# Performance work log

Hardware: AMD Instinct MI355X
Metric: run time of the kernel (lower is better)

## Reference

```python
import jax, jax.numpy as jnp
import numpy as np

N_NODES = 100000
N_EDGES = 1600000
IN_FEATS = 128
N_HIDDEN = 128
N_CLASSES = 47


def setup_inputs() -> dict:
    key = jax.random.key(0)
    ks = jax.random.split(key, 12)
    def lin(k, fi, fo):
        s = 1.0 / np.sqrt(fi)
        return jax.random.uniform(k, (fi, fo), jnp.float32, -s, s)
    return {
        "x": jax.random.normal(ks[0], (N_NODES, IN_FEATS), jnp.float32),
        "src": jax.random.randint(ks[1], (N_EDGES,), 0, N_NODES, jnp.int32),
        "dst": jax.random.randint(ks[2], (N_EDGES,), 0, N_NODES, jnp.int32),
        "W_self0": lin(ks[3], IN_FEATS, N_HIDDEN),
        "W_neigh0": lin(ks[4], IN_FEATS, N_HIDDEN),
        "b0": jnp.zeros((N_HIDDEN,), jnp.float32),
        "W_self1": lin(ks[5], N_HIDDEN, N_HIDDEN),
        "W_neigh1": lin(ks[6], N_HIDDEN, N_HIDDEN),
        "b1": jnp.zeros((N_HIDDEN,), jnp.float32),
        "W_self2": lin(ks[7], N_HIDDEN, N_CLASSES),
        "W_neigh2": lin(ks[8], N_HIDDEN, N_CLASSES),
        "b2": jnp.zeros((N_CLASSES,), jnp.float32),
    }


def _sage_layer(h, src, dst, W_self, W_neigh, b):
    # DGL SAGEConv 'mean': fc_self(h_dst) + fc_neigh(mean of in-neighbor feats) + bias
    agg = jax.ops.segment_sum(h[src], dst, num_segments=N_NODES)  # [N, d]
    deg = jax.ops.segment_sum(jnp.ones((src.shape[0],), h.dtype), dst,
                              num_segments=N_NODES)
    h_neigh = agg / jnp.maximum(deg, 1.0)[:, None]
    return h @ W_self + h_neigh @ W_neigh + b


def reference(x, src, dst, W_self0, W_neigh0, b0, W_self1, W_neigh1, b1,
              W_self2, W_neigh2, b2):
    h = _sage_layer(x, src, dst, W_self0, W_neigh0, b0)
    h = jax.nn.relu(h)
    h = _sage_layer(h, src, dst, W_self1, W_neigh1, b1)
    h = jax.nn.relu(h)
    h = _sage_layer(h, src, dst, W_self2, W_neigh2, b2)
    return h
```

## Files before the change

### kernel.cpp

```cpp
#include <hip/hip_runtime.h>

#define NN 100000
#define NE 1600000
#define NBK 391
#define CHUNK 8192
#define NBLK ((NE + CHUNK - 1) / CHUNK)
#define MPAD 100096
#define NCAST4 (NN * 32)
#define CAST512 (NCAST4 / 512)
#define GBLK 2048
#define NPW ((NN + 8191) / 8192)

using bf16x8 = __attribute__((ext_vector_type(8))) short;
using f32x4  = __attribute__((ext_vector_type(4))) float;

static __device__ __forceinline__ unsigned short f2bf(float f) {
    unsigned int u = __float_as_uint(f);
    unsigned int r = (u + 0x7FFFu + ((u >> 16) & 1u)) >> 16;
    return (unsigned short)r;
}
static __device__ __forceinline__ float lo16(unsigned int u) {
    return __uint_as_float(u << 16);
}
static __device__ __forceinline__ float hi16(unsigned int u) {
    return __uint_as_float(u & 0xFFFF0000u);
}
static __device__ __forceinline__ unsigned int pk(float lo, float hi) {
    return ((unsigned int)f2bf(hi) << 16) | (unsigned int)f2bf(lo);
}


__global__ __launch_bounds__(256) void k_hist(const int* __restrict__ dst,
                                              int* __restrict__ ghist) {
    __shared__ int h[NBK];
    int b = blockIdx.x, t = threadIdx.x;
    for (int i = t; i < NBK; i += 256) h[i] = 0;
    __syncthreads();
    int beg = b * CHUNK, end = min(beg + CHUNK, NE);
    for (int i = beg + t; i < end; i += 256)
        atomicAdd(&h[dst[i] >> 8], 1);
    __syncthreads();
    for (int i = t; i < NBK; i += 256) ghist[b * NBK + i] = h[i];
}

__global__ __launch_bounds__(512) void k_basescan_prep(
        const int* __restrict__ ghist, int* __restrict__ boff, int* __restrict__ gbase,
        const float4* __restrict__ x4, ushort4* __restrict__ XB4,
        const float* __restrict__ Ws0, const float* __restrict__ Wn0,
        unsigned short* __restrict__ BT0,
        const float* __restrict__ Ws1, const float* __restrict__ Wn1,
        unsigned short* __restrict__ BT1,
        const float* __restrict__ Ws2, const float* __restrict__ Wn2,
        unsigned short* __restrict__ BT2) {
    __shared__ int s[512];
    int bid = blockIdx.x, t = threadIdx.x;
    if (bid == 0) {
        int tot = 0;
        if (t < NBK) {
#pragma unroll 4
            for (int blk = 0; blk < NBLK; ++blk) tot += ghist[blk * NBK + t];
        }
        s[t] = tot;
        __syncthreads();
        for (int o = 1; o < 512; o <<= 1) {
            int u = (t >= o) ? s[t - o] : 0;
            __syncthreads();
            s[t] += u;
            __syncthreads();
        }
        int base = s[t] - tot;
        if (t <= NBK) boff[t] = base;
        if (t < NBK) {
            int run = base;
            for (int blk = 0; blk < NBLK; ++blk) {
                int g = ghist[blk * NBK + t];
                gbase[blk * NBK + t] = run;
                run += g;
            }
        }
        return;
    }
    int pb = bid - 1;
    if (pb < CAST512) {
        int i = pb * 512 + t;
        float4 v = x4[i];
        ushort4 o;
        o.x = f2bf(v.x); o.y = f2bf(v.y); o.z = f2bf(v.z); o.w = f2bf(v.w);
        XB4[i] = o;
    } else if (pb < CAST512 + 64) {
        int idx = (pb - CAST512) * 512 + t;
        int k = idx >> 7, n = idx & 127;
        float v = (k < 128) ? Ws0[k * 128 + n] : Wn0[(k - 128) * 128 + n];
        BT0[n * 256 + k] = f2bf(v);
    } else if (pb < CAST512 + 128) {
        int idx = (pb - CAST512 - 64) * 512 + t;
        int k = idx >> 7, n = idx & 127;
        float v = (k < 128) ? Ws1[k * 128 + n] : Wn1[(k - 128) * 128 + n];
        BT1[n * 256 + k] = f2bf(v);
    } else {
        int idx = (pb - CAST512 - 128) * 512 + t;
        if (idx < 96 * 128) {
            int n = idx >> 7, k = idx & 127;
            float v = 0.f;
            if (n < 48) { if (n < 47) v = Ws2[k * 47 + n]; }
            else        { int cc = n - 48; if (cc < 47) v = Wn2[k * 47 + cc]; }
            BT2[n * 128 + k] = f2bf(v);
        }
    }
}

__global__ __launch_bounds__(256) void k_scatter(const int* __restrict__ src,
                                                 const int* __restrict__ dst,
                                                 const int* __restrict__ gbase,
                                                 unsigned int* __restrict__ eb) {
    __shared__ int cur[NBK];
    int b = blockIdx.x, t = threadIdx.x;
    for (int i = t; i < NBK; i += 256) cur[i] = gbase[b * NBK + i];
    __syncthreads();
    int beg = b * CHUNK, end = min(beg + CHUNK, NE);
    for (int i = beg + t; i < end; i += 256) {
        int d = dst[i];
        int p = atomicAdd(&cur[d >> 8], 1);
        eb[p] = ((unsigned int)(d & 255) << 24) | (unsigned int)src[i];
    }
}

__global__ __launch_bounds__(256) void k_csr(const unsigned int* __restrict__ eb,
                                             const int* __restrict__ boff,
                                             int* __restrict__ rp,
                                             int* __restrict__ col) {
    __shared__ int h[256];
    __shared__ int sc[256];
    __shared__ int cur[256];
    int b = blockIdx.x, t = threadIdx.x;
    h[t] = 0;
    __syncthreads();
    int beg = boff[b], end = boff[b + 1];
    for (int e = beg + t; e < end; e += 256)
        atomicAdd(&h[eb[e] >> 24], 1);
    __syncthreads();
    int c = h[t];
    sc[t] = c;
    __syncthreads();
    for (int o = 1; o < 256; o <<= 1) {
        int v = (t >= o) ? sc[t - o] : 0;
        __syncthreads();
        sc[t] += v;
        __syncthreads();
    }
    int excl = beg + sc[t] - c;
    int node = (b << 8) + t;
    if (node < NN) rp[node] = excl;
    if (node == NN - 1) rp[NN] = NE;
    cur[t] = excl;
    __syncthreads();
    for (int e = beg + t; e < end; e += 256) {
        unsigned int p = eb[e];
        int pos = atomicAdd(&cur[p >> 24], 1);
        col[pos] = (int)(p & 0xFFFFFFu);
    }
}


__global__ __launch_bounds__(256) void k_gather128(
        const uint4* __restrict__ hb4,
        const int* __restrict__ rp, const int* __restrict__ col,
        uint4* __restrict__ hnb4) {
    int wave = blockIdx.x * 4 + (threadIdx.x >> 6);
    int lane = threadIdx.x & 63;
    int q = lane >> 4, l16 = lane & 15;
    int n0 = wave * NPW;
    int n1 = min(n0 + NPW, NN);
    for (int node = n0; node < n1; ++node) {
        int beg = rp[node], end = rp[node + 1];
        float a0 = 0.f, a1 = 0.f, a2 = 0.f, a3 = 0.f;
        float a4 = 0.f, a5 = 0.f, a6 = 0.f, a7 = 0.f;
        float b0 = 0.f, b1 = 0.f, b2 = 0.f, b3 = 0.f;
        float b4 = 0.f, b5 = 0.f, b6 = 0.f, b7 = 0.f;
        int e = beg;
        for (; e + 8 <= end; e += 8) {
            int c0 = col[e + q];
            int c1 = col[e + 4 + q];
            uint4 v0 = hb4[(size_t)c0 * 16 + l16];
            uint4 v1 = hb4[(size_t)c1 * 16 + l16];
            a0 += lo16(v0.x); a1 += hi16(v0.x); a2 += lo16(v0.y); a3 += hi16(v0.y);
            a4 += lo16(v0.z); a5 += hi16(v0.z); a6 += lo16(v0.w); a7 += hi16(v0.w);
            b0 += lo16(v1.x); b1 += hi16(v1.x); b2 += lo16(v1.y); b3 += hi16(v1.y);
            b4 += lo16(v1.z); b5 += hi16(v1.z); b6 += lo16(v1.w); b7 += hi16(v1.w);
        }
        for (; e < end; e += 4) {
            if (e + q < end) {
                uint4 v = hb4[(size_t)col[e + q] * 16 + l16];
                a0 += lo16(v.x); a1 += hi16(v.x); a2 += lo16(v.y); a3 += hi16(v.y);
                a4 += lo16(v.z); a5 += hi16(v.z); a6 += lo16(v.w); a7 += hi16(v.w);
            }
        }
        float s0 = a0 + b0, s1 = a1 + b1, s2 = a2 + b2, s3 = a3 + b3;
        float s4 = a4 + b4, s5 = a5 + b5, s6 = a6 + b6, s7 = a7 + b7;
        s0 += __shfl_xor(s0, 16); s0 += __shfl_xor(s0, 32);
        s1 += __shfl_xor(s1, 16); s1 += __shfl_xor(s1, 32);
        s2 += __shfl_xor(s2, 16); s2 += __shfl_xor(s2, 32);
        s3 += __shfl_xor(s3, 16); s3 += __shfl_xor(s3, 32);
        s4 += __shfl_xor(s4, 16); s4 += __shfl_xor(s4, 32);
        s5 += __shfl_xor(s5, 16); s5 += __shfl_xor(s5, 32);
        s6 += __shfl_xor(s6, 16); s6 += __shfl_xor(s6, 32);
        s7 += __shfl_xor(s7, 16); s7 += __shfl_xor(s7, 32);
        if (q == 0) {
            float d = (float)(end - beg);
            float inv = (d > 0.f) ? 1.0f / d : 0.0f;
            uint4 o;
            o.x = pk(s0 * inv, s1 * inv);
            o.y = pk(s2 * inv, s3 * inv);
            o.z = pk(s4 * inv, s5 * inv);
            o.w = pk(s6 * inv, s7 * inv);
            hnb4[(size_t)node * 16 + l16] = o;
        }
    }
}


__global__ __launch_bounds__(256, 2) void k_mgemm(
        const unsigned short* __restrict__ A0,
        const unsigned short* __restrict__ A1,
        const unsigned short* __restrict__ BT,
        const float* __restrict__ bias,
        unsigned short* __restrict__ outB) {
    int t = threadIdx.x;
    int lane = t & 63, wid = t >> 6;
    int wm = wid >> 1, wn = wid & 1;
    int lr = lane & 15, lg = lane >> 4;
    int row0 = blockIdx.x * 128 + wm * 64;
    int colw = wn * 64;
    f32x4 zero = {0.f, 0.f, 0.f, 0.f};
    f32x4 acc[4][4];
#pragma unroll
    for (int a = 0; a < 4; ++a)
#pragma unroll
        for (int b = 0; b < 4; ++b) acc[a][b] = zero;

#pragma unroll
    for (int p = 0; p < 2; ++p) {
        const unsigned short* A = p ? A1 : A0;
        bf16x8 bReg[4][4];
#pragma unroll
        for (int nf = 0; nf < 4; ++nf)
#pragma unroll
            for (int ks = 0; ks < 4; ++ks)
                bReg[nf][ks] = *(const bf16x8*)&BT[(size_t)(colw + nf * 16 + lr) * 256 + p * 128 + ks * 32 + lg * 8];
#pragma unroll
        for (int mf = 0; mf < 4; ++mf) {
            const unsigned short* Ar = A + (size_t)(row0 + mf * 16 + lr) * 128;
            bf16x8 aReg[4];
#pragma unroll
            for (int ks = 0; ks < 4; ++ks)
                aReg[ks] = *(const bf16x8*)&Ar[ks * 32 + lg * 8];
#pragma unroll
            for (int ks = 0; ks < 4; ++ks)
#pragma unroll
                for (int nf = 0; nf < 4; ++nf)
                    acc[mf][nf] = __builtin_amdgcn_mfma_f32_16x16x32_bf16(
                        aReg[ks], bReg[nf][ks], acc[mf][nf], 0, 0, 0);
        }
    }
    __syncthreads();
#pragma unroll
    for (int nf = 0; nf < 4; ++nf) {
        int cidx = colw + nf * 16 + lr;
        float bb = bias[cidx];
#pragma unroll
        for (int mf = 0; mf < 4; ++mf) {
#pragma unroll
            for (int j = 0; j < 4; ++j) {
                int row = row0 + mf * 16 + lg * 4 + j;
                if (row < NN) {
                    float v = fmaxf(acc[mf][nf][j] + bb, 0.f);
                    outB[(size_t)row * 128 + cidx] = f2bf(v);
                }
            }
        }
    }
}


__global__ __launch_bounds__(256, 2) void k_mgemm47(
        const unsigned short* __restrict__ A,
        const unsigned short* __restrict__ BT2,
        const float* __restrict__ bias,
        float* __restrict__ S,
        unsigned short* __restrict__ TB) {
    int t = threadIdx.x;
    int lane = t & 63, wid = t >> 6;
    int wm = wid >> 1, wn = wid & 1;
    int lr = lane & 15, lg = lane >> 4;
    int row0 = blockIdx.x * 128 + wm * 64;
    int colw = wn * 48;
    f32x4 zero = {0.f, 0.f, 0.f, 0.f};
    f32x4 acc[4][3];
#pragma unroll
    for (int a = 0; a < 4; ++a)
#pragma unroll
        for (int b = 0; b < 3; ++b) acc[a][b] = zero;

    bf16x8 bReg[3][4];
#pragma unroll
    for (int nf = 0; nf < 3; ++nf)
#pragma unroll
        for (int ks = 0; ks < 4; ++ks)
            bReg[nf][ks] = *(const bf16x8*)&BT2[(size_t)(colw + nf * 16 + lr) * 128 + ks * 32 + lg * 8];
#pragma unroll
    for (int mf = 0; mf < 4; ++mf) {
        const unsigned short* Ar = A + (size_t)(row0 + mf * 16 + lr) * 128;
        bf16x8 aReg[4];
#pragma unroll
        for (int ks = 0; ks < 4; ++ks)
            aReg[ks] = *(const bf16x8*)&Ar[ks * 32 + lg * 8];
#pragma unroll
        for (int ks = 0; ks < 4; ++ks)
#pragma unroll
            for (int nf = 0; nf < 3; ++nf)
                acc[mf][nf] = __builtin_amdgcn_mfma_f32_16x16x32_bf16(
                    aReg[ks], bReg[nf][ks], acc[mf][nf], 0, 0, 0);
    }
#pragma unroll
    for (int nf = 0; nf < 3; ++nf) {
        int cidx = colw + nf * 16 + lr;
#pragma unroll
        for (int mf = 0; mf < 4; ++mf) {
#pragma unroll
            for (int j = 0; j < 4; ++j) {
                int row = row0 + mf * 16 + lg * 4 + j;
                if (row < NN) {
                    float v = acc[mf][nf][j];
                    if (cidx < 47)
                        S[(size_t)row * 48 + cidx] = v + bias[cidx];
                    else if (cidx >= 48)
                        TB[(size_t)row * 64 + (cidx - 48)] = f2bf(v);
                }
            }
        }
    }
}


__global__ __launch_bounds__(256) void k_gather47(
        const uint2* __restrict__ TB2,
        const float4* __restrict__ S4,
        const int* __restrict__ rp, const int* __restrict__ col,
        float* __restrict__ out) {
    int wave = blockIdx.x * 4 + (threadIdx.x >> 6);
    int lane = threadIdx.x & 63;
    int q = lane >> 4, l16 = lane & 15;
    int n0 = wave * NPW;
    int n1 = min(n0 + NPW, NN);
    for (int node = n0; node < n1; ++node) {
        int beg = rp[node], end = rp[node + 1];
        float a0 = 0.f, a1 = 0.f, a2 = 0.f, a3 = 0.f;
        float b0 = 0.f, b1 = 0.f, b2 = 0.f, b3 = 0.f;
        int e = beg;
        for (; e + 8 <= end; e += 8) {
            int i0 = col[e + q];
            int i1 = col[e + 4 + q];
            uint2 u0 = TB2[(size_t)i0 * 16 + l16];
            uint2 u1 = TB2[(size_t)i1 * 16 + l16];
            a0 += lo16(u0.x); a1 += hi16(u0.x); a2 += lo16(u0.y); a3 += hi16(u0.y);
            b0 += lo16(u1.x); b1 += hi16(u1.x); b2 += lo16(u1.y); b3 += hi16(u1.y);
        }
        for (; e < end; e += 4) {
            if (e + q < end) {
                uint2 u = TB2[(size_t)col[e + q] * 16 + l16];
                a0 += lo16(u.x); a1 += hi16(u.x); a2 += lo16(u.y); a3 += hi16(u.y);
            }
        }
        float s0 = a0 + b0, s1 = a1 + b1, s2 = a2 + b2, s3 = a3 + b3;
        s0 += __shfl_xor(s0, 16); s0 += __shfl_xor(s0, 32);
        s1 += __shfl_xor(s1, 16); s1 += __shfl_xor(s1, 32);
        s2 += __shfl_xor(s2, 16); s2 += __shfl_xor(s2, 32);
        s3 += __shfl_xor(s3, 16); s3 += __shfl_xor(s3, 32);
        if (q == 0 && l16 < 12) {
            float d = (float)(end - beg);
            float inv = (d > 0.f) ? 1.0f / d : 0.0f;
            float4 sv = S4[(size_t)node * 12 + l16];
            int c = l16 * 4;
            out[(size_t)node * 47 + c]     = sv.x + s0 * inv;
            out[(size_t)node * 47 + c + 1] = sv.y + s1 * inv;
            out[(size_t)node * 47 + c + 2] = sv.z + s2 * inv;
            if (c + 3 < 47) out[(size_t)node * 47 + c + 3] = sv.w + s3 * inv;
        }
    }
}


static inline size_t align_up(size_t x, size_t a) { return (x + a - 1) / a * a; }

extern "C" void kernel_launch(void* const* d_in, const int* in_sizes, int n_in,
                              void* d_out, int out_size, void* d_ws, size_t ws_size,
                              hipStream_t stream) {
    const float* x   = (const float*)d_in[0];
    const int* src   = (const int*)d_in[1];
    const int* dst   = (const int*)d_in[2];
    const float* Ws0 = (const float*)d_in[3];
    const float* Wn0 = (const float*)d_in[4];
    const float* b0  = (const float*)d_in[5];
    const float* Ws1 = (const float*)d_in[6];
    const float* Wn1 = (const float*)d_in[7];
    const float* b1  = (const float*)d_in[8];
    const float* Ws2 = (const float*)d_in[9];
    const float* Wn2 = (const float*)d_in[10];
    const float* b2  = (const float*)d_in[11];
    float* out = (float*)d_out;

    char* ws = (char*)d_ws;
    size_t off = 0;
    auto alloc = [&](size_t bytes) -> void* {
        void* p = ws + off; off = align_up(off + bytes, 256); return p;
    };
    int* row_ptr = (int*)alloc((size_t)(NN + 1) * 4);
    int* boff    = (int*)alloc((size_t)(NBK + 1) * 4);
    int* gbase   = (int*)alloc((size_t)NBLK * NBK * 4);
    int* ghist   = (int*)alloc((size_t)NBLK * NBK * 4);
    int* col     = (int*)alloc((size_t)NE * 4);
    unsigned short* XB  = (unsigned short*)alloc((size_t)MPAD * 128 * 2);
    unsigned short* BT0 = (unsigned short*)alloc(128 * 256 * 2);
    unsigned short* BT1 = (unsigned short*)alloc(128 * 256 * 2);
    unsigned short* BT2 = (unsigned short*)alloc(96 * 128 * 2);
    size_t sbytes  = (size_t)NN * 48 * 4;
    size_t tbbytes = (size_t)MPAD * 64 * 2;
    size_t hnbytes = (size_t)MPAD * 128 * 2;
    size_t bigsz = sbytes + tbbytes;
    if (hnbytes > bigsz) bigsz = hnbytes;
    char* big = (char*)alloc(bigsz);
    unsigned int* eb    = (unsigned int*)big;
    unsigned int* HNB   = (unsigned int*)big;
    float* S            = (float*)big;
    unsigned short* TB  = (unsigned short*)(big + sbytes);

    k_hist<<<NBLK, 256, 0, stream>>>(dst, ghist);
    k_basescan_prep<<<1 + CAST512 + 128 + 24, 512, 0, stream>>>(
        ghist, boff, gbase,
        (const float4*)x, (ushort4*)XB, Ws0, Wn0, BT0, Ws1, Wn1, BT1, Ws2, Wn2, BT2);
    k_scatter<<<NBLK, 256, 0, stream>>>(src, dst, gbase, eb);
    k_csr<<<NBK, 256, 0, stream>>>(eb, boff, row_ptr, col);

    int mgrid = MPAD / 128;

    k_gather128<<<GBLK, 256, 0, stream>>>((const uint4*)XB, row_ptr, col, (uint4*)HNB);
    k_mgemm<<<mgrid, 256, 0, stream>>>(XB, (const unsigned short*)HNB, BT0, b0, XB);
    k_gather128<<<GBLK, 256, 0, stream>>>((const uint4*)XB, row_ptr, col, (uint4*)HNB);
    k_mgemm<<<mgrid, 256, 0, stream>>>(XB, (const unsigned short*)HNB, BT1, b1, XB);
    k_mgemm47<<<mgrid, 256, 0, stream>>>(XB, BT2, b2, S, TB);
    k_gather47<<<GBLK, 256, 0, stream>>>((const uint2*)TB, (const float4*)S,
                                         row_ptr, col, out);
}
```

Before: 353.2 us.

## Fuse layer-1 GEMM with layer-2 projection and merge histogram with prep casts

Merges the edge histogram kernel with the input/weight bf16 cast blocks into one launch, and moves the base scan into its own small kernel afterward. Fuses the layer-1 SAGE GEMM with the layer-2 projection GEMM by staging the ReLU'd bf16 hidden tile in shared memory and feeding it straight into the 47-class MFMA, which avoids re-reading the hidden activations from global memory and saves one launch. HNB now gets its own buffer instead of aliasing S/TB, which costs extra workspace. The fused kernel uses more registers and LDS, which may lower occupancy.

```diff
diff --git a/kernel.cpp b/kernel.cpp
--- a/kernel.cpp
+++ b/kernel.cpp
@@ -6,8 +6,8 @@
 #define CHUNK 8192
 #define NBLK ((NE + CHUNK - 1) / CHUNK)
 #define MPAD 100096
-#define NCAST4 (NN * 32)
-#define CAST512 (NCAST4 / 512)
+#define CASTB 12500
+#define PREPB (CASTB + 128 + 128 + 48)
 #define GBLK 2048
 #define NPW ((NN + 8191) / 8192)
 
@@ -30,21 +30,8 @@
 }
 
 
-__global__ __launch_bounds__(256) void k_hist(const int* __restrict__ dst,
-                                              int* __restrict__ ghist) {
-    __shared__ int h[NBK];
-    int b = blockIdx.x, t = threadIdx.x;
-    for (int i = t; i < NBK; i += 256) h[i] = 0;
-    __syncthreads();
-    int beg = b * CHUNK, end = min(beg + CHUNK, NE);
-    for (int i = beg + t; i < end; i += 256)
-        atomicAdd(&h[dst[i] >> 8], 1);
-    __syncthreads();
-    for (int i = t; i < NBK; i += 256) ghist[b * NBK + i] = h[i];
-}
-
-__global__ __launch_bounds__(512) void k_basescan_prep(
-        const int* __restrict__ ghist, int* __restrict__ boff, int* __restrict__ gbase,
+__global__ __launch_bounds__(256) void k_hist_prep(
+        const int* __restrict__ dst, int* __restrict__ ghist,
         const float4* __restrict__ x4, ushort4* __restrict__ XB4,
         const float* __restrict__ Ws0, const float* __restrict__ Wn0,
         unsigned short* __restrict__ BT0,
@@ -52,59 +39,73 @@
         unsigned short* __restrict__ BT1,
         const float* __restrict__ Ws2, const float* __restrict__ Wn2,
         unsigned short* __restrict__ BT2) {
-    __shared__ int s[512];
+    __shared__ int h[NBK];
     int bid = blockIdx.x, t = threadIdx.x;
-    if (bid == 0) {
-        int tot = 0;
-        if (t < NBK) {
-#pragma unroll 4
-            for (int blk = 0; blk < NBLK; ++blk) tot += ghist[blk * NBK + t];
-        }
-        s[t] = tot;
+    if (bid < NBLK) {
+        for (int i = t; i < NBK; i += 256) h[i] = 0;
         __syncthreads();
-        for (int o = 1; o < 512; o <<= 1) {
-            int u = (t >= o) ? s[t - o] : 0;
-            __syncthreads();
-            s[t] += u;
-            __syncthreads();
-        }
-        int base = s[t] - tot;
-        if (t <= NBK) boff[t] = base;
-        if (t < NBK) {
-            int run = base;
-            for (int blk = 0; blk < NBLK; ++blk) {
-                int g = ghist[blk * NBK + t];
-                gbase[blk * NBK + t] = run;
-                run += g;
-            }
-        }
+        int beg = bid * CHUNK, end = min(beg + CHUNK, NE);
+        for (int i = beg + t; i < end; i += 256)
+            atomicAdd(&h[dst[i] >> 8], 1);
+        __syncthreads();
+        for (int i = t; i < NBK; i += 256) ghist[bid * NBK + i] = h[i];
         return;
     }
-    int pb = bid - 1;
-    if (pb < CAST512) {
-        int i = pb * 512 + t;
+    int pb = bid - NBLK;
+    if (pb < CASTB) {
+        int i = pb * 256 + t;
         float4 v = x4[i];
         ushort4 o;
         o.x = f2bf(v.x); o.y = f2bf(v.y); o.z = f2bf(v.z); o.w = f2bf(v.w);
         XB4[i] = o;
-    } else if (pb < CAST512 + 64) {
-        int idx = (pb - CAST512) * 512 + t;
+    } else if (pb < CASTB + 128) {
+        int idx = (pb - CASTB) * 256 + t;
         int k = idx >> 7, n = idx & 127;
         float v = (k < 128) ? Ws0[k * 128 + n] : Wn0[(k - 128) * 128 + n];
         BT0[n * 256 + k] = f2bf(v);
-    } else if (pb < CAST512 + 128) {
-        int idx = (pb - CAST512 - 64) * 512 + t;
+    } else if (pb < CASTB + 256) {
+        int idx = (pb - CASTB - 128) * 256 + t;
         int k = idx >> 7, n = idx & 127;
         float v = (k < 128) ? Ws1[k * 128 + n] : Wn1[(k - 128) * 128 + n];
         BT1[n * 256 + k] = f2bf(v);
     } else {
-        int idx = (pb - CAST512 - 128) * 512 + t;
+        int idx = (pb - CASTB - 256) * 256 + t;
         if (idx < 96 * 128) {
             int n = idx >> 7, k = idx & 127;
             float v = 0.f;
             if (n < 48) { if (n < 47) v = Ws2[k * 47 + n]; }
             else        { int cc = n - 48; if (cc < 47) v = Wn2[k * 47 + cc]; }
             BT2[n * 128 + k] = f2bf(v);
+        }
+    }
+}
+
+__global__ __launch_bounds__(512) void k_basescan(const int* __restrict__ ghist,
+                                                  int* __restrict__ boff,
+                                                  int* __restrict__ gbase) {
+    __shared__ int s[512];
+    int t = threadIdx.x;
+    int tot = 0;
+    if (t < NBK) {
+#pragma unroll 4
+        for (int blk = 0; blk < NBLK; ++blk) tot += ghist[blk * NBK + t];
+    }
+    s[t] = tot;
+    __syncthreads();
+    for (int o = 1; o < 512; o <<= 1) {
+        int u = (t >= o) ? s[t - o] : 0;
+        __syncthreads();
+        s[t] += u;
+        __syncthreads();
+    }
+    int base = s[t] - tot;
+    if (t <= NBK) boff[t] = base;
+    if (t < NBK) {
+        int run = base;
+        for (int blk = 0; blk < NBLK; ++blk) {
+            int g = ghist[blk * NBK + t];
+            gbase[blk * NBK + t] = run;
+            run += g;
         }
     }
 }
@@ -282,57 +283,123 @@
 }
 
 
-__global__ __launch_bounds__(256, 2) void k_mgemm47(
-        const unsigned short* __restrict__ A,
+__global__ __launch_bounds__(256, 2) void k_mgemm_l12(
+        const unsigned short* __restrict__ A0,
+        const unsigned short* __restrict__ A1,
+        const unsigned short* __restrict__ BT,
+        const float* __restrict__ bias,
+        unsigned short* __restrict__ outB,
         const unsigned short* __restrict__ BT2,
-        const float* __restrict__ bias,
+        const float* __restrict__ bias2,
         float* __restrict__ S,
         unsigned short* __restrict__ TB) {
+    __shared__ unsigned short hl[128][132];
     int t = threadIdx.x;
     int lane = t & 63, wid = t >> 6;
     int wm = wid >> 1, wn = wid & 1;
     int lr = lane & 15, lg = lane >> 4;
     int row0 = blockIdx.x * 128 + wm * 64;
-    int colw = wn * 48;
+    int colw = wn * 64;
     f32x4 zero = {0.f, 0.f, 0.f, 0.f};
-    f32x4 acc[4][3];
+    f32x4 acc[4][4];
 #pragma unroll
     for (int a = 0; a < 4; ++a)
 #pragma unroll
-        for (int b = 0; b < 3; ++b) acc[a][b] = zero;
-
-    bf16x8 bReg[3][4];
+        for (int b = 0; b < 4; ++b) acc[a][b] = zero;
+
+#pragma unroll
+    for (int p = 0; p < 2; ++p) {
+        const unsigned short* A = p ? A1 : A0;
+        bf16x8 bReg[4][4];
+#pragma unroll
+        for (int nf = 0; nf < 4; ++nf)
+#pragma unroll
+            for (int ks = 0; ks < 4; ++ks)
+                bReg[nf][ks] = *(const bf16x8*)&BT[(size_t)(colw + nf * 16 + lr) * 256 + p * 128 + ks * 32 + lg * 8];
+#pragma unroll
+        for (int mf = 0; mf < 4; ++mf) {
+            const unsigned short* Ar = A + (size_t)(row0 + mf * 16 + lr) * 128;
+            bf16x8 aReg[4];
+#pragma unroll
+            for (int ks = 0; ks < 4; ++ks)
+                aReg[ks] = *(const bf16x8*)&Ar[ks * 32 + lg * 8];
+#pragma unroll
+            for (int ks = 0; ks < 4; ++ks)
+#pragma unroll
+                for (int nf = 0; nf < 4; ++nf)
+                    acc[mf][nf] = __builtin_amdgcn_mfma_f32_16x16x32_bf16(
+                        aReg[ks], bReg[nf][ks], acc[mf][nf], 0, 0, 0);
+        }
+    }
+#pragma unroll
+    for (int nf = 0; nf < 4; ++nf) {
+        int cidx = colw + nf * 16 + lr;
+        float bb = bias[cidx];
+#pragma unroll
+        for (int mf = 0; mf < 4; ++mf) {
+#pragma unroll
+            for (int j = 0; j < 4; ++j) {
+                int lrow = wm * 64 + mf * 16 + lg * 4 + j;
+                float v = fmaxf(acc[mf][nf][j] + bb, 0.f);
+                unsigned short bv = f2bf(v);
+                hl[lrow][cidx] = bv;
+                acc[mf][nf][j] = __uint_as_float((unsigned int)bv);
+            }
+        }
+    }
+    __syncthreads();
+#pragma unroll
+    for (int nf = 0; nf < 4; ++nf) {
+        int cidx = colw + nf * 16 + lr;
+#pragma unroll
+        for (int mf = 0; mf < 4; ++mf) {
+#pragma unroll
+            for (int j = 0; j < 4; ++j) {
+                int row = row0 + mf * 16 + lg * 4 + j;
+                if (row < NN)
+                    outB[(size_t)row * 128 + cidx] =
+                        (unsigned short)__float_as_uint(acc[mf][nf][j]);
+            }
+        }
+    }
+    int colw2 = wn * 48;
+    f32x4 acc2[4][3];
+#pragma unroll
+    for (int a = 0; a < 4; ++a)
+#pragma unroll
+        for (int b = 0; b < 3; ++b) acc2[a][b] = zero;
+    bf16x8 bReg2[3][4];
 #pragma unroll
     for (int nf = 0; nf < 3; ++nf)
 #pragma unroll
         for (int ks = 0; ks < 4; ++ks)
-            bReg[nf][ks] = *(const bf16x8*)&BT2[(size_t)(colw + nf * 16 + lr) * 128 + ks * 32 + lg * 8];
+            bReg2[nf][ks] = *(const bf16x8*)&BT2[(size_t)(colw2 + nf * 16 + lr) * 128 + ks * 32 + lg * 8];
 #pragma unroll
     for (int mf = 0; mf < 4; ++mf) {
-        const unsigned short* Ar = A + (size_t)(row0 + mf * 16 + lr) * 128;
+        int ar = wm * 64 + mf * 16 + lr;
         bf16x8 aReg[4];
 #pragma unroll
         for (int ks = 0; ks < 4; ++ks)
-            aReg[ks] = *(const bf16x8*)&Ar[ks * 32 + lg * 8];
+            aReg[ks] = *(const bf16x8*)&hl[ar][ks * 32 + lg * 8];
 #pragma unroll
         for (int ks = 0; ks < 4; ++ks)
 #pragma unroll
             for (int nf = 0; nf < 3; ++nf)
-                acc[mf][nf] = __builtin_amdgcn_mfma_f32_16x16x32_bf16(
-                    aReg[ks], bReg[nf][ks], acc[mf][nf], 0, 0, 0);
+                acc2[mf][nf] = __builtin_amdgcn_mfma_f32_16x16x32_bf16(
+                    aReg[ks], bReg2[nf][ks], acc2[mf][nf], 0, 0, 0);
     }
 #pragma unroll
     for (int nf = 0; nf < 3; ++nf) {
-        int cidx = colw + nf * 16 + lr;
+        int cidx = colw2 + nf * 16 + lr;
 #pragma unroll
         for (int mf = 0; mf < 4; ++mf) {
 #pragma unroll
             for (int j = 0; j < 4; ++j) {
                 int row = row0 + mf * 16 + lg * 4 + j;
                 if (row < NN) {
-                    float v = acc[mf][nf][j];
+                    float v = acc2[mf][nf][j];
                     if (cidx < 47)
-                        S[(size_t)row * 48 + cidx] = v + bias[cidx];
+                        S[(size_t)row * 48 + cidx] = v + bias2[cidx];
                     else if (cidx >= 48)
                         TB[(size_t)row * 64 + (cidx - 48)] = f2bf(v);
                 }
@@ -423,21 +490,18 @@
     unsigned short* BT0 = (unsigned short*)alloc(128 * 256 * 2);
     unsigned short* BT1 = (unsigned short*)alloc(128 * 256 * 2);
     unsigned short* BT2 = (unsigned short*)alloc(96 * 128 * 2);
+    unsigned int* HNB   = (unsigned int*)alloc((size_t)MPAD * 128 * 2);
     size_t sbytes  = (size_t)NN * 48 * 4;
     size_t tbbytes = (size_t)MPAD * 64 * 2;
-    size_t hnbytes = (size_t)MPAD * 128 * 2;
-    size_t bigsz = sbytes + tbbytes;
-    if (hnbytes > bigsz) bigsz = hnbytes;
-    char* big = (char*)alloc(bigsz);
-    unsigned int* eb    = (unsigned int*)big;
-    unsigned int* HNB   = (unsigned int*)big;
-    float* S            = (float*)big;
-    unsigned short* TB  = (unsigned short*)(big + sbytes);
-
-    k_hist<<<NBLK, 256, 0, stream>>>(dst, ghist);
-    k_basescan_prep<<<1 + CAST512 + 128 + 24, 512, 0, stream>>>(
-        ghist, boff, gbase,
-        (const float4*)x, (ushort4*)XB, Ws0, Wn0, BT0, Ws1, Wn1, BT1, Ws2, Wn2, BT2);
+    char* stb = (char*)alloc(sbytes + tbbytes);
+    unsigned int* eb   = (unsigned int*)stb;
+    float* S           = (float*)stb;
+    unsigned short* TB = (unsigned short*)(stb + sbytes);
+
+    k_hist_prep<<<NBLK + PREPB, 256, 0, stream>>>(
+        dst, ghist, (const float4*)x, (ushort4*)XB,
+        Ws0, Wn0, BT0, Ws1, Wn1, BT1, Ws2, Wn2, BT2);
+    k_basescan<<<1, 512, 0, stream>>>(ghist, boff, gbase);
     k_scatter<<<NBLK, 256, 0, stream>>>(src, dst, gbase, eb);
     k_csr<<<NBK, 256, 0, stream>>>(eb, boff, row_ptr, col);
 
@@ -446,8 +510,8 @@
     k_gather128<<<GBLK, 256, 0, stream>>>((const uint4*)XB, row_ptr, col, (uint4*)HNB);
     k_mgemm<<<mgrid, 256, 0, stream>>>(XB, (const unsigned short*)HNB, BT0, b0, XB);
     k_gather128<<<GBLK, 256, 0, stream>>>((const uint4*)XB, row_ptr, col, (uint4*)HNB);
-    k_mgemm<<<mgrid, 256, 0, stream>>>(XB, (const unsigned short*)HNB, BT1, b1, XB);
-    k_mgemm47<<<mgrid, 256, 0, stream>>>(XB, BT2, b2, S, TB);
+    k_mgemm_l12<<<mgrid, 256, 0, stream>>>(XB, (const unsigned short*)HNB, BT1, b1, XB,
+                                           BT2, b2, S, TB);
     k_gather47<<<GBLK, 256, 0, stream>>>((const uint2*)TB, (const float4*)S,
                                          row_ptr, col, out);
 }
```

Measured after the change: 343.8 us. 1.03x faster.
